# Performance work log

Hardware: AMD Instinct MI355X
Metric: run time of the kernel (lower is better)

Reference implementation:

```python
import jax, jax.numpy as jnp
import numpy as np

H = 96
NH = 4
HD = H // NH
SPARSITY = 0.5
LN_EPS = 1e-5


def _lstm_layer(xs, w_ih, w_hh, b_ih, b_hh):
    # xs: [B, T, I]; PyTorch gate order i, f, g, o
    B = xs.shape[0]
    Hd = w_hh.shape[1]
    def step(carry, x_t):
        h, c = carry
        gates = x_t @ w_ih.T + h @ w_hh.T + b_ih + b_hh  # [B, 4H]
        i, f, g, o = jnp.split(gates, 4, axis=-1)
        i = jax.nn.sigmoid(i); f = jax.nn.sigmoid(f)
        g = jnp.tanh(g); o = jax.nn.sigmoid(o)
        c = f * c + i * g
        h = o * jnp.tanh(c)
        return (h, c), h
    h0 = jnp.zeros((B, Hd), xs.dtype)
    c0 = jnp.zeros((B, Hd), xs.dtype)
    _, hs = jax.lax.scan(step, (h0, c0), xs.transpose(1, 0, 2))  # [T, B, H]
    return hs.transpose(1, 0, 2)


def _layer_norm(x, w, b):
    mu = jnp.mean(x, axis=-1, keepdims=True)
    var = jnp.mean((x - mu) ** 2, axis=-1, keepdims=True)
    return (x - mu) * jax.lax.rsqrt(var + LN_EPS) * w + b


def _split_heads(x, B, T):
    return x.reshape(B, T, NH, HD).transpose(0, 2, 1, 3)  # [B, H, T, d]


def _sparse_attention(x, qw, kw, vw, ow):
    B, T, _ = x.shape
    q = _split_heads(x @ qw.T, B, T)
    k = _split_heads(x @ kw.T, B, T)
    v = _split_heads(x @ vw.T, B, T)
    scores = jnp.einsum('bhtd,bhsd->bhts', q, k) / np.sqrt(HD).astype(np.float32)
    num_keep = int(T * SPARSITY)
    topv, _ = jax.lax.top_k(scores, num_keep)
    kth = topv[..., -1:]  # threshold == k-th largest (equiv to topk+scatter mask for distinct values)
    scores = jnp.where(scores >= kth, scores, -jnp.inf)
    attn = jax.nn.softmax(scores, axis=-1)  # dropout is identity in eval
    out = jnp.einsum('bhts,bhsd->bhtd', attn, v)
    out = out.transpose(0, 2, 1, 3).reshape(B, T, H)
    return out @ ow.T


def _mha(x, in_w, in_b, out_w, out_b):
    B, T, _ = x.shape
    qkv = x @ in_w.T + in_b  # [B, T, 3H]
    q, k, v = jnp.split(qkv, 3, axis=-1)
    q = _split_heads(q, B, T); k = _split_heads(k, B, T); v = _split_heads(v, B, T)
    scores = jnp.einsum('bhtd,bhsd->bhts', q, k) / np.sqrt(HD).astype(np.float32)
    attn = jax.nn.softmax(scores, axis=-1)
    out = jnp.einsum('bhts,bhsd->bhtd', attn, v)
    out = out.transpose(0, 2, 1, 3).reshape(B, T, H)
    return out @ out_w.T + out_b


def _encoder_layer(x, in_w, in_b, out_w, out_b, l1_w, l1_b, l2_w, l2_b, ln1_w, ln1_b, ln2_w, ln2_b):
    # PyTorch TransformerEncoderLayer, post-norm, ReLU, eval (no dropout)
    x = _layer_norm(x + _mha(x, in_w, in_b, out_w, out_b), ln1_w, ln1_b)
    ff = jax.nn.relu(x @ l1_w.T + l1_b) @ l2_w.T + l2_b
    return _layer_norm(x + ff, ln2_w, ln2_b)


def setup_inputs() -> dict:
    key = jax.random.key(0)
    ks = iter(jax.random.split(key, 40))
    B, T, I = 16, 1024, 64
    FF = 2 * H
    def rnd(shape, scale=0.05):
        return (jax.random.normal(next(ks), shape, dtype=jnp.float32) * scale)
    inp = {
        'x': jax.random.normal(next(ks), (B, T, I), dtype=jnp.float32),
        'w_ih0': rnd((4 * H, I)), 'w_hh0': rnd((4 * H, H)),
        'b_ih0': rnd((4 * H,)), 'b_hh0': rnd((4 * H,)),
        'w_ih1': rnd((4 * H, H)), 'w_hh1': rnd((4 * H, H)),
        'b_ih1': rnd((4 * H,)), 'b_hh1': rnd((4 * H,)),
        'qw': rnd((H, H)), 'kw': rnd((H, H)), 'vw': rnd((H, H)), 'ow': rnd((H, H)),
        'enc_in_w': rnd((2, 3 * H, H)), 'enc_in_b': rnd((2, 3 * H)),
        'enc_out_w': rnd((2, H, H)), 'enc_out_b': rnd((2, H)),
        'enc_l1_w': rnd((2, FF, H)), 'enc_l1_b': rnd((2, FF)),
        'enc_l2_w': rnd((2, H, FF)), 'enc_l2_b': rnd((2, H)),
        'enc_ln1_w': jnp.ones((2, H), jnp.float32), 'enc_ln1_b': jnp.zeros((2, H), jnp.float32),
        'enc_ln2_w': jnp.ones((2, H), jnp.float32), 'enc_ln2_b': jnp.zeros((2, H), jnp.float32),
        'fc_w': rnd((1, H)), 'fc_b': rnd((1,)),
    }
    return inp


def reference(x, w_ih0, w_hh0, b_ih0, b_hh0, w_ih1, w_hh1, b_ih1, b_hh1,
              qw, kw, vw, ow,
              enc_in_w, enc_in_b, enc_out_w, enc_out_b,
              enc_l1_w, enc_l1_b, enc_l2_w, enc_l2_b,
              enc_ln1_w, enc_ln1_b, enc_ln2_w, enc_ln2_b,
              fc_w, fc_b):
    h = _lstm_layer(x, w_ih0, w_hh0, b_ih0, b_hh0)
    h = _lstm_layer(h, w_ih1, w_hh1, b_ih1, b_hh1)
    h = _sparse_attention(h, qw, kw, vw, ow)
    for i in range(2):
        h = _encoder_layer(h, enc_in_w[i], enc_in_b[i], enc_out_w[i], enc_out_b[i],
                           enc_l1_w[i], enc_l1_b[i], enc_l2_w[i], enc_l2_b[i],
                           enc_ln1_w[i], enc_ln1_b[i], enc_ln2_w[i], enc_ln2_b[i])
    return h[:, -1, :] @ fc_w.T + fc_b  # [B, 1]
```

## Files before the change

kernel.cpp:

```cpp
#include <hip/hip_runtime.h>
#include <cstdint>
#include <cmath>

#define T_SEQ 1024
#define BATCH 16
#define HID 96
#define G4 384
#define QKV_LD 288
#define HDIM 24
#define KKEEP 512
#define SCALE 0.20412414523193154f
#define L2E 1.4426950408889634f

typedef _Float16 half2v __attribute__((ext_vector_type(2)));
typedef __bf16 bf16x8 __attribute__((ext_vector_type(8)));
typedef float  f32x4v __attribute__((ext_vector_type(4)));

__device__ __forceinline__ float wred_sum(float v){
#pragma unroll
  for (int o=32;o;o>>=1) v += __shfl_xor(v,o,64);
  return v;
}
__device__ __forceinline__ float wred_max(float v){
#pragma unroll
  for (int o=32;o;o>>=1) v = fmaxf(v,__shfl_xor(v,o,64));
  return v;
}
__device__ __forceinline__ unsigned fmono(float f){
  unsigned u = __float_as_uint(f);
  return (u & 0x80000000u) ? ~u : (u | 0x80000000u);
}
__device__ __forceinline__ float sigf(float x){
  return __builtin_amdgcn_rcpf(1.f + __builtin_amdgcn_exp2f(-L2E*x));
}
__device__ __forceinline__ float tanhf2(float x){
  return fmaf(-2.f, __builtin_amdgcn_rcpf(1.f + __builtin_amdgcn_exp2f((2.f*L2E)*x)), 1.f);
}
template<int CTRL>
__device__ __forceinline__ float dpp_add_f(float v){
  int s = __builtin_amdgcn_update_dpp(0, __float_as_int(v), CTRL, 0xF, 0xF, true);
  return v + __int_as_float(s);
}
__device__ __forceinline__ float dpp_red4(float v){
  v = dpp_add_f<0xB1>(v);
  v = dpp_add_f<0x4E>(v);
  return v;
}
#if __has_builtin(__builtin_amdgcn_fdot2)
__device__ __forceinline__ float fdot2(half2v a, half2v b, float c){
  return __builtin_amdgcn_fdot2(a, b, c, false);
}
#else
__device__ __forceinline__ float fdot2(half2v a, half2v b, float c){
  return fmaf((float)a[0], (float)b[0], fmaf((float)a[1], (float)b[1], c));
}
#endif
__device__ __forceinline__ half2v pkh2(float a, float b){
  return __builtin_bit_cast(half2v, __builtin_amdgcn_cvt_pkrtz(a, b));
}
__device__ __forceinline__ unsigned short f2bf(float f){
  unsigned u = __float_as_uint(f);
  return (unsigned short)((u + 0x7fffu + ((u>>16)&1u)) >> 16);
}
__device__ __forceinline__ f32x4v mfma16(uint4 a, uint4 b, f32x4v c){
  return __builtin_amdgcn_mfma_f32_16x16x32_bf16(
      __builtin_bit_cast(bf16x8, a), __builtin_bit_cast(bf16x8, b), c, 0, 0, 0);
}

template<int K>
__global__ __launch_bounds__(256)
void gemm_mfma(const float* __restrict__ A, const float* __restrict__ W,
               const float* __restrict__ b1, const float* __restrict__ b2,
               float* __restrict__ C, int N, int ldc, int coff, int relu)
{
  __shared__ unsigned short As[128][K+8];
  __shared__ unsigned short Ws[64][K+8];
  const int tid = threadIdx.x;
  const int wave = tid >> 6, lane = tid & 63;
  const int ln = lane & 15, kq = lane >> 4;
  const int m0 = blockIdx.y * 128, n0 = blockIdx.x * 64;

  for (int idx = tid; idx < 128*(K/4); idx += 256){
    const int row = idx / (K/4), c4 = idx - row*(K/4);
    const float4 v = *(const float4*)(A + (size_t)(m0+row)*K + c4*4);
    ushort4 s = {f2bf(v.x), f2bf(v.y), f2bf(v.z), f2bf(v.w)};
    *(ushort4*)&As[row][c4*4] = s;
  }
  for (int idx = tid; idx < 64*(K/4); idx += 256){
    const int row = idx / (K/4), c4 = idx - row*(K/4);
    float4 v = {0,0,0,0};
    const int gn = n0 + row;
    if (gn < N) v = *(const float4*)(W + (size_t)gn*K + c4*4);
    ushort4 s = {f2bf(v.x), f2bf(v.y), f2bf(v.z), f2bf(v.w)};
    *(ushort4*)&Ws[row][c4*4] = s;
  }
  __syncthreads();

  f32x4v acc[2][4];
#pragma unroll
  for (int mi=0;mi<2;++mi)
#pragma unroll
    for (int ni=0;ni<4;++ni){ f32x4v z = {0.f,0.f,0.f,0.f}; acc[mi][ni] = z; }

#pragma unroll
  for (int ks=0; ks<K/32; ++ks){
    uint4 af[2], bf[4];
#pragma unroll
    for (int mi=0;mi<2;++mi)
      af[mi] = *(const uint4*)&As[wave*32 + mi*16 + ln][ks*32 + kq*8];
#pragma unroll
    for (int ni=0;ni<4;++ni)
      bf[ni] = *(const uint4*)&Ws[ni*16 + ln][ks*32 + kq*8];
#pragma unroll
    for (int mi=0;mi<2;++mi)
#pragma unroll
      for (int ni=0;ni<4;++ni)
        acc[mi][ni] = mfma16(af[mi], bf[ni], acc[mi][ni]);
  }

#pragma unroll
  for (int ni=0;ni<4;++ni){
    const int gn = n0 + ni*16 + ln;
    if (gn >= N) continue;
    float bias = 0.f;
    if (b1) bias += b1[gn];
    if (b2) bias += b2[gn];
#pragma unroll
    for (int mi=0;mi<2;++mi){
      const int row = m0 + wave*32 + mi*16 + kq*4;
#pragma unroll
      for (int r=0;r<4;++r){
        float v = acc[mi][ni][r] + bias;
        if (relu) v = fmaxf(v, 0.f);
        C[(size_t)(row + r)*ldc + coff + gn] = v;
      }
    }
  }
}

__global__ __launch_bounds__(256)
void pack_qkv_kernel(const float* __restrict__ qw, const float* __restrict__ kw,
                     const float* __restrict__ vw, float* __restrict__ wqkv)
{
  const int i = blockIdx.x*256 + threadIdx.x;
  if (i < 9216)       wqkv[i] = qw[i];
  else if (i < 18432) wqkv[i] = kw[i-9216];
  else if (i < 27648) wqkv[i] = vw[i-18432];
}

__global__ __launch_bounds__(384)
void lstm_kernel(const float* __restrict__ pre, const float* __restrict__ w_hh,
                 float* __restrict__ hout)
{
  const int b = blockIdx.x;
  const int tid = threadIdx.x;
  const int q = tid & 3, j = tid >> 2;
  half2v w[4][12];
#pragma unroll
  for (int g=0; g<4; ++g){
    const float* wp = w_hh + (size_t)(g*96 + j)*96 + q*24;
#pragma unroll
    for (int k=0;k<12;++k){
      half2v t; t[0] = (_Float16)wp[2*k]; t[1] = (_Float16)wp[2*k+1];
      w[g][k] = t;
    }
  }
  __shared__ _Float16 h_lds[96];
  float c = 0.f;
  if (tid < 96) h_lds[tid] = (_Float16)0.f;
  __syncthreads();

  const float* prow = pre + (size_t)b*T_SEQ*G4 + q*96 + j;
  float* hrow = hout + (size_t)b*T_SEQ*HID;
  float pf[4];
#pragma unroll
  for (int i=0;i<4;++i) pf[i] = prow[(size_t)i*G4];
  float hv_prev = 0.f;

  for (int tb=0; tb<T_SEQ; tb+=4){
#pragma unroll
    for (int u=0; u<4; ++u){
      const int t = tb + u;
      if (q == 0 && t > 0)
        hrow[(size_t)(t-1)*HID + j] = hv_prev;
      const float pcur = pf[u];
      int tn = t + 4; if (tn > T_SEQ-1) tn = T_SEQ-1;
      pf[u] = prow[(size_t)tn*G4];
      const uint4 a0 = *(const uint4*)(h_lds + q*24);
      const uint4 a1 = *(const uint4*)(h_lds + q*24 + 8);
      const uint4 a2 = *(const uint4*)(h_lds + q*24 + 16);
      half2v h2[12];
      h2[0]=__builtin_bit_cast(half2v, a0.x); h2[1]=__builtin_bit_cast(half2v, a0.y);
      h2[2]=__builtin_bit_cast(half2v, a0.z); h2[3]=__builtin_bit_cast(half2v, a0.w);
      h2[4]=__builtin_bit_cast(half2v, a1.x); h2[5]=__builtin_bit_cast(half2v, a1.y);
      h2[6]=__builtin_bit_cast(half2v, a1.z); h2[7]=__builtin_bit_cast(half2v, a1.w);
      h2[8]=__builtin_bit_cast(half2v, a2.x); h2[9]=__builtin_bit_cast(half2v, a2.y);
      h2[10]=__builtin_bit_cast(half2v, a2.z); h2[11]=__builtin_bit_cast(half2v, a2.w);

      float sA0=0.f,sA1=0.f,sA2=0.f,sA3=0.f;
      float sB0=0.f,sB1=0.f,sB2=0.f,sB3=0.f;
#pragma unroll
      for (int k=0;k<12;k+=2){
        sA0 = fdot2(w[0][k], h2[k], sA0);  sB0 = fdot2(w[0][k+1], h2[k+1], sB0);
        sA1 = fdot2(w[1][k], h2[k], sA1);  sB1 = fdot2(w[1][k+1], h2[k+1], sB1);
        sA2 = fdot2(w[2][k], h2[k], sA2);  sB2 = fdot2(w[2][k+1], h2[k+1], sB2);
        sA3 = fdot2(w[3][k], h2[k], sA3);  sB3 = fdot2(w[3][k+1], h2[k+1], sB3);
      }
      float s0 = sA0+sB0, s1 = sA1+sB1, s2 = sA2+sB2, s3 = sA3+sB3;
      s0 += (q==0) ? pcur : 0.f;
      s1 += (q==1) ? pcur : 0.f;
      s2 += (q==2) ? pcur : 0.f;
      s3 += (q==3) ? pcur : 0.f;
      s0 = dpp_red4(s0);
      s1 = dpp_red4(s1);
      s2 = dpp_red4(s2);
      s3 = dpp_red4(s3);
      const float iv = sigf(s0), fv = sigf(s1);
      const float gv = tanhf2(s2), ov = sigf(s3);
      c = fmaf(fv, c, iv*gv);
      const float hv = ov * tanhf2(c);
      if (q == 0){
        h_lds[j] = (_Float16)hv;
        hv_prev = hv;
      }
      __syncthreads();
    }
  }
  if (q == 0)
    hrow[(size_t)(T_SEQ-1)*HID + j] = hv_prev;
}

__global__ __launch_bounds__(512, 1)
void attn_kernel(const float* __restrict__ qkv, float* __restrict__ out, int sparse)
{
  __shared__ float kl[24][260];
  unsigned* klh = (unsigned*)&kl[0][0];
  const int tid = threadIdx.x;
  const int wave = tid >> 6, lane = tid & 63;
  const int bh = blockIdx.x >> 6;
  const int b = bh >> 2, h = bh & 3;
  const int tq = ((blockIdx.x & 63) << 4) + wave*2;
  const size_t base = (size_t)b * T_SEQ;
  const int hoff = h * HDIM;
  half2v q20[12], q21[12];
  {
    const float* qp0 = qkv + (base + tq)*QKV_LD + hoff;
    const float* qp1 = qp0 + QKV_LD;
#pragma unroll
    for (int d4=0; d4<6; ++d4){
      float4 t0 = *(const float4*)(qp0 + d4*4);
      float4 t1 = *(const float4*)(qp1 + d4*4);
      q20[d4*2+0] = pkh2(t0.x, t0.y); q20[d4*2+1] = pkh2(t0.z, t0.w);
      q21[d4*2+0] = pkh2(t1.x, t1.y); q21[d4*2+1] = pkh2(t1.z, t1.w);
    }
  }
  float sc0[16], sc1[16];
  for (int c=0;c<4;++c){
    __syncthreads();
#pragma unroll
    for (int rep=0;rep<3;++rep){
      int p = rep*512 + tid;
      int sl = p/6, d4 = p - sl*6;
      const float4 kv = *(const float4*)(qkv + (base + (c<<8) + sl)*QKV_LD + 96 + hoff + d4*4);
      klh[(d4*2+0)*260 + sl] = __builtin_bit_cast(unsigned, pkh2(kv.x, kv.y));
      klh[(d4*2+1)*260 + sl] = __builtin_bit_cast(unsigned, pkh2(kv.z, kv.w));
    }
    __syncthreads();
    float a0=0.f,a1=0.f,a2=0.f,a3=0.f;
    float b0=0.f,b1v=0.f,b2v=0.f,b3=0.f;
#pragma unroll
    for (int dp=0; dp<12; ++dp){
      const uint4 kd = *(const uint4*)&klh[dp*260 + lane*4];
      const half2v k0 = __builtin_bit_cast(half2v, kd.x);
      const half2v k1 = __builtin_bit_cast(half2v, kd.y);
      const half2v k2 = __builtin_bit_cast(half2v, kd.z);
      const half2v k3 = __builtin_bit_cast(half2v, kd.w);
      a0 = fdot2(q20[dp], k0, a0); a1 = fdot2(q20[dp], k1, a1);
      a2 = fdot2(q20[dp], k2, a2); a3 = fdot2(q20[dp], k3, a3);
      b0 = fdot2(q21[dp], k0, b0); b1v = fdot2(q21[dp], k1, b1v);
      b2v = fdot2(q21[dp], k2, b2v); b3 = fdot2(q21[dp], k3, b3);
    }
    sc0[c*4+0]=a0*SCALE; sc0[c*4+1]=a1*SCALE; sc0[c*4+2]=a2*SCALE; sc0[c*4+3]=a3*SCALE;
    sc1[c*4+0]=b0*SCALE; sc1[c*4+1]=b1v*SCALE; sc1[c*4+2]=b2v*SCALE; sc1[c*4+3]=b3*SCALE;
  }
  float inv0, inv1;
#define SOFTMAX_ROW(SC, INV)                                                  \
  {                                                                           \
    float m_loc = SC[0];                                                      \
    _Pragma("unroll")                                                         \
    for (int i=1;i<16;++i) m_loc = fmaxf(m_loc, SC[i]);                       \
    const float m = wred_max(m_loc);                                          \
    float sum_loc = 0.f;                                                      \
    if (sparse){                                                              \
      unsigned u[16];                                                         \
      _Pragma("unroll")                                                       \
      for (int i=0;i<16;++i) u[i] = fmono(SC[i]);                             \
      unsigned prefix = 0;                                                    \
      for (int bit=31; bit>=0; --bit){                                        \
        const unsigned test = prefix | (1u<<bit);                             \
        int cnt = 0;                                                          \
        _Pragma("unroll")                                                     \
        for (int i=0;i<16;++i)                                                \
          cnt += (int)__popcll(__ballot(u[i] >= test));                       \
        if (cnt >= KKEEP) prefix = test;                                      \
      }                                                                       \
      _Pragma("unroll")                                                       \
      for (int i=0;i<16;++i){                                                 \
        float e = (u[i] >= prefix) ? __expf(SC[i]-m) : 0.f;                   \
        SC[i] = e; sum_loc += e;                                              \
      }                                                                       \
    } else {                                                                  \
      _Pragma("unroll")                                                       \
      for (int i=0;i<16;++i){                                                 \
        float e = __expf(SC[i]-m);                                            \
        SC[i] = e; sum_loc += e;                                              \
      }                                                                       \
    }                                                                         \
    INV = 1.f / wred_sum(sum_loc);                                            \
  }
  SOFTMAX_ROW(sc0, inv0)
  SOFTMAX_ROW(sc1, inv1)
#undef SOFTMAX_ROW
#pragma unroll
  for (int i=0;i<16;++i){ sc0[i] *= inv0; sc1[i] *= inv1; }
  float acc0[24] = {}, acc1[24] = {};
  for (int c=0;c<4;++c){
    __syncthreads();
#pragma unroll
    for (int rep=0;rep<3;++rep){
      int p = rep*512 + tid;
      int sl = p/6, d4 = p - sl*6;
      const float4 vv = *(const float4*)(qkv + (base + (c<<8) + sl)*QKV_LD + 192 + hoff + d4*4);
      kl[d4*4+0][sl]=vv.x; kl[d4*4+1][sl]=vv.y; kl[d4*4+2][sl]=vv.z; kl[d4*4+3][sl]=vv.w;
    }
    __syncthreads();
    const float w00=sc0[c*4], w01=sc0[c*4+1], w02=sc0[c*4+2], w03=sc0[c*4+3];
    const float w10=sc1[c*4], w11=sc1[c*4+1], w12=sc1[c*4+2], w13=sc1[c*4+3];
#pragma unroll
    for (int d=0; d<24; ++d){
      const float4 vd = *(const float4*)&kl[d][lane*4];
      acc0[d] += w00*vd.x + w01*vd.y + w02*vd.z + w03*vd.w;
      acc1[d] += w10*vd.x + w11*vd.y + w12*vd.z + w13*vd.w;
    }
  }
#pragma unroll
  for (int d=0; d<24; ++d){ acc0[d] = wred_sum(acc0[d]); acc1[d] = wred_sum(acc1[d]); }
  if (lane == 0){
    float* op0 = out + (base + tq)*HID + hoff;
    float* op1 = op0 + HID;
#pragma unroll
    for (int d4=0; d4<6; ++d4){
      float4 t0 = {acc0[d4*4], acc0[d4*4+1], acc0[d4*4+2], acc0[d4*4+3]};
      float4 t1 = {acc1[d4*4], acc1[d4*4+1], acc1[d4*4+2], acc1[d4*4+3]};
      *(float4*)(op0 + d4*4) = t0;
      *(float4*)(op1 + d4*4) = t1;
    }
  }
}

__global__ __launch_bounds__(64)
void attn_last_kernel(const float* __restrict__ qkv, float* __restrict__ out)
{
  const int bh = blockIdx.x, b = bh>>2, h = bh&3;
  const int lane = threadIdx.x;
  const size_t base = (size_t)b*T_SEQ;
  const int hoff = h*HDIM;
  float q[24];
  {
    const float* qp = qkv + (base + T_SEQ-1)*QKV_LD + hoff;
#pragma unroll
    for (int d4=0; d4<6; ++d4){
      float4 t = *(const float4*)(qp + d4*4);
      q[d4*4]=t.x; q[d4*4+1]=t.y; q[d4*4+2]=t.z; q[d4*4+3]=t.w;
    }
  }
  float sc[16];
#pragma unroll 4
  for (int i=0;i<16;++i){
    const float* kp = qkv + (base + i*64 + lane)*QKV_LD + 96 + hoff;
    float a = 0.f;
#pragma unroll
    for (int d4=0; d4<6; ++d4){
      float4 kv = *(const float4*)(kp + d4*4);
      a += q[d4*4]*kv.x + q[d4*4+1]*kv.y + q[d4*4+2]*kv.z + q[d4*4+3]*kv.w;
    }
    sc[i] = a*SCALE;
  }
  float m_loc = sc[0];
#pragma unroll
  for (int i=1;i<16;++i) m_loc = fmaxf(m_loc, sc[i]);
  const float m = wred_max(m_loc);
  float sum_loc = 0.f;
#pragma unroll
  for (int i=0;i<16;++i){ sc[i] = __expf(sc[i]-m); sum_loc += sc[i]; }
  const float inv = 1.f / wred_sum(sum_loc);
  float acc[24] = {};
#pragma unroll 4
  for (int i=0;i<16;++i){
    const float* vp = qkv + (base + i*64 + lane)*QKV_LD + 192 + hoff;
    const float wgt = sc[i]*inv;
#pragma unroll
    for (int d4=0; d4<6; ++d4){
      float4 vv = *(const float4*)(vp + d4*4);
      acc[d4*4]   += wgt*vv.x; acc[d4*4+1] += wgt*vv.y;
      acc[d4*4+2] += wgt*vv.z; acc[d4*4+3] += wgt*vv.w;
    }
  }
#pragma unroll
  for (int d=0; d<24; ++d) acc[d] = wred_sum(acc[d]);
  if (lane == 0){
    float* op = out + (base + T_SEQ-1)*HID + hoff;
#pragma unroll
    for (int d4=0; d4<6; ++d4){
      float4 t = {acc[d4*4], acc[d4*4+1], acc[d4*4+2], acc[d4*4+3]};
      *(float4*)(op + d4*4) = t;
    }
  }
}

__global__ __launch_bounds__(256)
void resln_kernel(const float* __restrict__ x, const float* __restrict__ y,
                  const float* __restrict__ w, const float* __restrict__ bb,
                  float* __restrict__ out)
{
  const int row = blockIdx.x*4 + (threadIdx.x>>6);
  const int lane = threadIdx.x & 63;
  const float* xr = x + (size_t)row*HID;
  const float* yr = y + (size_t)row*HID;
  float v0 = xr[lane] + yr[lane];
  float v1 = (lane < 32) ? (xr[64+lane] + yr[64+lane]) : 0.f;
  float mu = wred_sum(v0+v1) * (1.f/96.f);
  float d0 = v0-mu, d1 = (lane<32) ? (v1-mu) : 0.f;
  float var = wred_sum(d0*d0 + d1*d1) * (1.f/96.f);
  float rs = rsqrtf(var + 1e-5f);
  float* orow = out + (size_t)row*HID;
  orow[lane] = d0*rs*w[lane] + bb[lane];
  if (lane < 32) orow[64+lane] = d1*rs*w[64+lane] + bb[64+lane];
}

__device__ __forceinline__ float block_sum_192(float v, float* red){
  v = wred_sum(v);
  const int tid = threadIdx.x;
  if ((tid & 63) == 0) red[tid>>6] = v;
  __syncthreads();
  float r = red[0]+red[1]+red[2];
  __syncthreads();
  return r;
}

__global__ __launch_bounds__(192)
void tail_kernel(const float* __restrict__ xin, const float* __restrict__ mha,
                 const float* __restrict__ out_w, const float* __restrict__ out_b,
                 const float* __restrict__ l1_w, const float* __restrict__ l1_b,
                 const float* __restrict__ l2_w, const float* __restrict__ l2_b,
                 const float* __restrict__ ln1w, const float* __restrict__ ln1b,
                 const float* __restrict__ ln2w, const float* __restrict__ ln2b,
                 const float* __restrict__ fcw, const float* __restrict__ fcb,
                 float* __restrict__ outp)
{
  const int b = blockIdx.x, tid = threadIdx.x;
  __shared__ float y[96], f1[192], mrow[96], red[3];
  const size_t row = ((size_t)b*T_SEQ + T_SEQ-1)*HID;
  if (tid < 96) mrow[tid] = mha[row + tid];
  __syncthreads();
  float r = 0.f;
  if (tid < 96){
    float p = out_b[tid];
    const float* wr = out_w + tid*96;
#pragma unroll 4
    for (int d=0; d<96; ++d) p += mrow[d]*wr[d];
    r = xin[row + tid] + p;
  }
  float mu = block_sum_192(tid<96 ? r : 0.f, red) * (1.f/96.f);
  float dv = tid<96 ? r-mu : 0.f;
  float var = block_sum_192(dv*dv, red) * (1.f/96.f);
  float rs = rsqrtf(var + 1e-5f);
  if (tid < 96) y[tid] = dv*rs*ln1w[tid] + ln1b[tid];
  __syncthreads();
  {
    float a = l1_b[tid];
    const float* wr = l1_w + tid*96;
#pragma unroll 4
    for (int d=0; d<96; ++d) a += y[d]*wr[d];
    f1[tid] = fmaxf(a, 0.f);
  }
  __syncthreads();
  float r2 = 0.f;
  if (tid < 96){
    float a = l2_b[tid];
    const float* wr = l2_w + tid*192;
#pragma unroll 4
    for (int d=0; d<192; ++d) a += f1[d]*wr[d];
    r2 = y[tid] + a;
  }
  float mu2 = block_sum_192(tid<96 ? r2 : 0.f, red) * (1.f/96.f);
  float dv2 = tid<96 ? r2-mu2 : 0.f;
  float var2 = block_sum_192(dv2*dv2, red) * (1.f/96.f);
  float rs2 = rsqrtf(var2 + 1e-5f);
  float z = tid<96 ? (dv2*rs2*ln2w[tid] + ln2b[tid]) : 0.f;
  float tot = block_sum_192(tid<96 ? z*fcw[tid] : 0.f, red);
  if (tid == 0) outp[b] = tot + fcb[0];
}

extern "C" void kernel_launch(void* const* d_in, const int* in_sizes, int n_in,
                              void* d_out, int out_size, void* d_ws, size_t ws_size,
                              hipStream_t stream)
{
  const float* x     = (const float*)d_in[0];
  const float* w_ih0 = (const float*)d_in[1];
  const float* w_hh0 = (const float*)d_in[2];
  const float* b_ih0 = (const float*)d_in[3];
  const float* b_hh0 = (const float*)d_in[4];
  const float* w_ih1 = (const float*)d_in[5];
  const float* w_hh1 = (const float*)d_in[6];
  const float* b_ih1 = (const float*)d_in[7];
  const float* b_hh1 = (const float*)d_in[8];
  const float* qw = (const float*)d_in[9];
  const float* kw = (const float*)d_in[10];
  const float* vw = (const float*)d_in[11];
  const float* ow = (const float*)d_in[12];
  const float* enc_in_w  = (const float*)d_in[13];
  const float* enc_in_b  = (const float*)d_in[14];
  const float* enc_out_w = (const float*)d_in[15];
  const float* enc_out_b = (const float*)d_in[16];
  const float* enc_l1_w  = (const float*)d_in[17];
  const float* enc_l1_b  = (const float*)d_in[18];
  const float* enc_l2_w  = (const float*)d_in[19];
  const float* enc_l2_b  = (const float*)d_in[20];
  const float* enc_ln1_w = (const float*)d_in[21];
  const float* enc_ln1_b = (const float*)d_in[22];
  const float* enc_ln2_w = (const float*)d_in[23];
  const float* enc_ln2_b = (const float*)d_in[24];
  const float* fc_w = (const float*)d_in[25];
  const float* fc_b = (const float*)d_in[26];
  float* outp = (float*)d_out;

  float* ws = (float*)d_ws;
  const size_t MT = (size_t)BATCH*T_SEQ;
  float* pre  = ws;
  float* bufA = pre  + MT*G4;
  float* bufB = bufA + MT*HID;
  float* bufC = bufB + MT*HID;
  float* wqkv = bufC + MT*HID;

  auto gemm = [&](const float* A, const float* W, const float* bb1, const float* bb2,
                  float* C, int N, int K, int ldc, int coff, int relu){
    dim3 grid((N+63)/64, 128);
    if (K == 64)
      gemm_mfma<64><<<grid, dim3(256), 0, stream>>>(A, W, bb1, bb2, C, N, ldc, coff, relu);
    else if (K == 96)
      gemm_mfma<96><<<grid, dim3(256), 0, stream>>>(A, W, bb1, bb2, C, N, ldc, coff, relu);
    else
      gemm_mfma<192><<<grid, dim3(256), 0, stream>>>(A, W, bb1, bb2, C, N, ldc, coff, relu);
  };

  pack_qkv_kernel<<<dim3(108), dim3(256), 0, stream>>>(qw, kw, vw, wqkv);

  gemm(x, w_ih0, b_ih0, b_hh0, pre, 384, 64, 384, 0, 0);
  lstm_kernel<<<dim3(BATCH), dim3(384), 0, stream>>>(pre, w_hh0, bufA);
  gemm(bufA, w_ih1, b_ih1, b_hh1, pre, 384, 96, 384, 0, 0);
  lstm_kernel<<<dim3(BATCH), dim3(384), 0, stream>>>(pre, w_hh1, bufB);
  gemm(bufB, wqkv, nullptr, nullptr, pre, 288, 96, QKV_LD, 0, 0);
  attn_kernel<<<dim3(4096), dim3(512), 0, stream>>>(pre, bufA, 1);
  gemm(bufA, ow, nullptr, nullptr, bufB, 96, 96, 96, 0, 0);
  gemm(bufB, enc_in_w, enc_in_b, nullptr, pre, 288, 96, QKV_LD, 0, 0);
  attn_kernel<<<dim3(4096), dim3(512), 0, stream>>>(pre, bufA, 0);
  gemm(bufA, enc_out_w, enc_out_b, nullptr, bufC, 96, 96, 96, 0, 0);
  resln_kernel<<<dim3(4096), dim3(256), 0, stream>>>(bufB, bufC, enc_ln1_w, enc_ln1_b, bufB);
  gemm(bufB, enc_l1_w, enc_l1_b, nullptr, pre, 192, 96, 192, 0, 1);
  gemm(pre, enc_l2_w, enc_l2_b, nullptr, bufC, 96, 192, 96, 0, 0);
  resln_kernel<<<dim3(4096), dim3(256), 0, stream>>>(bufB, bufC, enc_ln2_w, enc_ln2_b, bufB);
  gemm(bufB, enc_in_w + 288*96, enc_in_b + 288, nullptr, pre, 288, 96, QKV_LD, 0, 0);
  attn_last_kernel<<<dim3(64), dim3(64), 0, stream>>>(pre, bufA);
  tail_kernel<<<dim3(BATCH), dim3(192), 0, stream>>>(
      bufB, bufA,
      enc_out_w + 96*96, enc_out_b + 96,
      enc_l1_w + 192*96, enc_l1_b + 192,
      enc_l2_w + 96*192, enc_l2_b + 96,
      enc_ln1_w + 96, enc_ln1_b + 96,
      enc_ln2_w + 96, enc_ln2_b + 96,
      fc_w, fc_b, outp);
}
```

Measured before the change: 1.816 ms.

## Double-buffer attention K/V tiles with register prefetch and lighter LDS barrier

In the attention kernel, K and V chunks are now prefetched into registers one chunk ahead and written into two alternating LDS buffers. This cuts the two barriers per chunk to one and hides global load latency behind the dot-product work. A custom barrier that waits only on LDS counters before s_barrier replaces __syncthreads in the LSTM recurrence and attention loops, so pending global memory operations no longer stall each step. The cost is a larger LDS footprint, more live registers, and a barrier that relies on no global-memory dependency existing across it.

Result: slower. 2.915 ms (+60.6%).

```diff
diff --git a/kernel.cpp b/kernel.cpp
--- a/kernel.cpp
+++ b/kernel.cpp
@@ -65,6 +65,10 @@
 __device__ __forceinline__ f32x4v mfma16(uint4 a, uint4 b, f32x4v c){
   return __builtin_amdgcn_mfma_f32_16x16x32_bf16(
       __builtin_bit_cast(bf16x8, a), __builtin_bit_cast(bf16x8, b), c, 0, 0, 0);
+}
+__device__ __forceinline__ void barrier_lds(){
+  asm volatile("s_waitcnt lgkmcnt(0)" ::: "memory");
+  __builtin_amdgcn_s_barrier();
 }
 
 template<int K>
@@ -223,7 +227,7 @@
         h_lds[j] = (_Float16)hv;
         hv_prev = hv;
       }
-      __syncthreads();
+      barrier_lds();
     }
   }
   if (q == 0)
@@ -233,8 +237,7 @@
 __global__ __launch_bounds__(512, 1)
 void attn_kernel(const float* __restrict__ qkv, float* __restrict__ out, int sparse)
 {
-  __shared__ float kl[24][260];
-  unsigned* klh = (unsigned*)&kl[0][0];
+  __shared__ float kl[2][24][260];
   const int tid = threadIdx.x;
   const int wave = tid >> 6, lane = tid & 63;
   const int bh = blockIdx.x >> 6;
@@ -242,6 +245,10 @@
   const int tq = ((blockIdx.x & 63) << 4) + wave*2;
   const size_t base = (size_t)b * T_SEQ;
   const int hoff = h * HDIM;
+  const int p0 = tid,        sl0 = p0/6, d40 = p0 - sl0*6;
+  const int p1 = 512 + tid,  sl1 = p1/6, d41 = p1 - sl1*6;
+  const int p2 = 1024 + tid, sl2 = p2/6, d42 = p2 - sl2*6;
+
   half2v q20[12], q21[12];
   {
     const float* qp0 = qkv + (base + tq)*QKV_LD + hoff;
@@ -255,22 +262,35 @@
     }
   }
   float sc0[16], sc1[16];
+
+#define LDQKV(C, SL, D4, KOFF) \
+  (*(const float4*)(qkv + (base + ((C)<<8) + (SL))*QKV_LD + (KOFF) + hoff + (D4)*4))
+
+  float4 rA0 = LDQKV(0, sl0, d40, 96);
+  float4 rA1 = LDQKV(0, sl1, d41, 96);
+  float4 rA2 = LDQKV(0, sl2, d42, 96);
+  float4 rB0 = rA0, rB1 = rA1, rB2 = rA2;
+#pragma unroll
   for (int c=0;c<4;++c){
-    __syncthreads();
-#pragma unroll
-    for (int rep=0;rep<3;++rep){
-      int p = rep*512 + tid;
-      int sl = p/6, d4 = p - sl*6;
-      const float4 kv = *(const float4*)(qkv + (base + (c<<8) + sl)*QKV_LD + 96 + hoff + d4*4);
-      klh[(d4*2+0)*260 + sl] = __builtin_bit_cast(unsigned, pkh2(kv.x, kv.y));
-      klh[(d4*2+1)*260 + sl] = __builtin_bit_cast(unsigned, pkh2(kv.z, kv.w));
-    }
-    __syncthreads();
+    unsigned* klhc = (unsigned*)&kl[c&1][0][0];
+    klhc[(d40*2+0)*260 + sl0] = __builtin_bit_cast(unsigned, pkh2(rA0.x, rA0.y));
+    klhc[(d40*2+1)*260 + sl0] = __builtin_bit_cast(unsigned, pkh2(rA0.z, rA0.w));
+    klhc[(d41*2+0)*260 + sl1] = __builtin_bit_cast(unsigned, pkh2(rA1.x, rA1.y));
+    klhc[(d41*2+1)*260 + sl1] = __builtin_bit_cast(unsigned, pkh2(rA1.z, rA1.w));
+    klhc[(d42*2+0)*260 + sl2] = __builtin_bit_cast(unsigned, pkh2(rA2.x, rA2.y));
+    klhc[(d42*2+1)*260 + sl2] = __builtin_bit_cast(unsigned, pkh2(rA2.z, rA2.w));
+    if (c < 3){
+      rB0 = LDQKV(c+1, sl0, d40, 96);
+      rB1 = LDQKV(c+1, sl1, d41, 96);
+      rB2 = LDQKV(c+1, sl2, d42, 96);
+    }
+    barrier_lds();
+    const unsigned* klr = (const unsigned*)&kl[c&1][0][0];
     float a0=0.f,a1=0.f,a2=0.f,a3=0.f;
     float b0=0.f,b1v=0.f,b2v=0.f,b3=0.f;
 #pragma unroll
     for (int dp=0; dp<12; ++dp){
-      const uint4 kd = *(const uint4*)&klh[dp*260 + lane*4];
+      const uint4 kd = *(const uint4*)&klr[dp*260 + lane*4];
       const half2v k0 = __builtin_bit_cast(half2v, kd.x);
       const half2v k1 = __builtin_bit_cast(half2v, kd.y);
       const half2v k2 = __builtin_bit_cast(half2v, kd.z);
@@ -282,7 +302,13 @@
     }
     sc0[c*4+0]=a0*SCALE; sc0[c*4+1]=a1*SCALE; sc0[c*4+2]=a2*SCALE; sc0[c*4+3]=a3*SCALE;
     sc1[c*4+0]=b0*SCALE; sc1[c*4+1]=b1v*SCALE; sc1[c*4+2]=b2v*SCALE; sc1[c*4+3]=b3*SCALE;
-  }
+    rA0 = rB0; rA1 = rB1; rA2 = rB2;
+  }
+
+  float4 vA0 = LDQKV(0, sl0, d40, 192);
+  float4 vA1 = LDQKV(0, sl1, d41, 192);
+  float4 vA2 = LDQKV(0, sl2, d42, 192);
+
   float inv0, inv1;
 #define SOFTMAX_ROW(SC, INV)                                                  \
   {                                                                           \
@@ -323,26 +349,35 @@
 #undef SOFTMAX_ROW
 #pragma unroll
   for (int i=0;i<16;++i){ sc0[i] *= inv0; sc1[i] *= inv1; }
+
   float acc0[24] = {}, acc1[24] = {};
+  float4 vB0 = vA0, vB1 = vA1, vB2 = vA2;
+#pragma unroll
   for (int c=0;c<4;++c){
-    __syncthreads();
-#pragma unroll
-    for (int rep=0;rep<3;++rep){
-      int p = rep*512 + tid;
-      int sl = p/6, d4 = p - sl*6;
-      const float4 vv = *(const float4*)(qkv + (base + (c<<8) + sl)*QKV_LD + 192 + hoff + d4*4);
-      kl[d4*4+0][sl]=vv.x; kl[d4*4+1][sl]=vv.y; kl[d4*4+2][sl]=vv.z; kl[d4*4+3][sl]=vv.w;
-    }
-    __syncthreads();
+    float (*klc)[260] = kl[c&1];
+    klc[d40*4+0][sl0]=vA0.x; klc[d40*4+1][sl0]=vA0.y;
+    klc[d40*4+2][sl0]=vA0.z; klc[d40*4+3][sl0]=vA0.w;
+    klc[d41*4+0][sl1]=vA1.x; klc[d41*4+1][sl1]=vA1.y;
+    klc[d41*4+2][sl1]=vA1.z; klc[d41*4+3][sl1]=vA1.w;
+    klc[d42*4+0][sl2]=vA2.x; klc[d42*4+1][sl2]=vA2.y;
+    klc[d42*4+2][sl2]=vA2.z; klc[d42*4+3][sl2]=vA2.w;
+    if (c < 3){
+      vB0 = LDQKV(c+1, sl0, d40, 192);
+      vB1 = LDQKV(c+1, sl1, d41, 192);
+      vB2 = LDQKV(c+1, sl2, d42, 192);
+    }
+    barrier_lds();
     const float w00=sc0[c*4], w01=sc0[c*4+1], w02=sc0[c*4+2], w03=sc0[c*4+3];
     const float w10=sc1[c*4], w11=sc1[c*4+1], w12=sc1[c*4+2], w13=sc1[c*4+3];
 #pragma unroll
     for (int d=0; d<24; ++d){
-      const float4 vd = *(const float4*)&kl[d][lane*4];
+      const float4 vd = *(const float4*)&kl[c&1][d][lane*4];
       acc0[d] += w00*vd.x + w01*vd.y + w02*vd.z + w03*vd.w;
       acc1[d] += w10*vd.x + w11*vd.y + w12*vd.z + w13*vd.w;
     }
-  }
+    vA0 = vB0; vA1 = vB1; vA2 = vB2;
+  }
+#undef LDQKV
 #pragma unroll
   for (int d=0; d<24; ++d){ acc0[d] = wred_sum(acc0[d]); acc1[d] = wred_sum(acc1[d]); }
   if (lane == 0){
```
